# Performance work log

Measured on AMD Instinct MI355X. Metric: run time of the kernel, lower is better.

The kernel has to match this reference:

```python
import jax, jax.numpy as jnp
import numpy as np

B, L = 4, 1024
V, D, H, NL = 32000, 256, 4, 8
S, DC, DI, NTYPES = 16, 4, 512, 5  # d_state, d_conv, d_inner=expand*d_model
NM, NA = 6, 2  # mamba blocks (layers 0,1,2,4,5,6), attention blocks (layers 3,7)


def layernorm(x, g, b):
    m = x.mean(-1, keepdims=True)
    v = x.var(-1, keepdims=True)
    return (x - m) / jnp.sqrt(v + 1e-5) * g + b


def mamba_block(x, g, b, in_w, conv_w, conv_b, xproj_w, dt_w, dt_b, A_log, Dp, out_w):
    res = x
    xn = layernorm(x, g, b)
    xz = xn @ in_w.T                          # [B,L,2*DI]
    xb, z = jnp.split(xz, 2, axis=-1)
    # depthwise causal conv1d (torch pads both sides then truncates to L == left-pad only)
    xc = jnp.transpose(xb, (0, 2, 1))         # [B,DI,L]
    xc = jax.lax.conv_general_dilated(xc, conv_w, (1,), [(DC - 1, 0)], feature_group_count=DI)
    xc = xc + conv_b[None, :, None]
    xb = jax.nn.silu(jnp.transpose(xc, (0, 2, 1)))  # [B,L,DI]
    A = -jnp.exp(A_log)                        # [DI,S]
    Bm, Cm = jnp.split(xb @ xproj_w.T, 2, axis=-1)  # each [B,L,S]
    dt = jax.nn.softplus(xb @ dt_w.T + dt_b)   # [B,L,DI]

    def step(h, inp):
        dt_t, B_t, C_t, x_t = inp              # [B,DI],[B,S],[B,S],[B,DI]
        A_bar = jnp.exp(dt_t[:, :, None] * A)  # [B,DI,S]
        h = A_bar * h + (dt_t * x_t)[:, :, None] * B_t[:, None, :]
        y = (h * C_t[:, None, :]).sum(-1) + Dp * x_t
        return h, y

    h0 = jnp.zeros((x.shape[0], DI, S), x.dtype)
    xs = (jnp.swapaxes(dt, 0, 1), jnp.swapaxes(Bm, 0, 1), jnp.swapaxes(Cm, 0, 1), jnp.swapaxes(xb, 0, 1))
    _, ys = jax.lax.scan(step, h0, xs)         # ys: [L,B,DI]
    y = jnp.swapaxes(ys, 0, 1) * jax.nn.silu(z)
    return y @ out_w.T + res


def attn_block(x, ts, mask, g, b, qkv_w, out_w, decay, ffg, ffb, ff1, ff2):
    Bs, Lq, Dm = x.shape
    dh = Dm // H
    res = x
    xn = layernorm(x, g, b)
    qkv = (xn @ qkv_w.T).reshape(Bs, Lq, 3, H, dh)
    q, k, v = qkv[:, :, 0], qkv[:, :, 1], qkv[:, :, 2]   # [B,L,H,dh]
    attn = jnp.einsum('bqhd,bkhd->bhqk', q, k) * dh ** -0.5
    t_diff = jnp.abs(ts[:, :, None] - ts[:, None, :])[:, None] / 24.0   # [B,1,L,L]
    attn = attn - jax.nn.softplus(decay)[None, :, None, None] * t_diff
    causal = jnp.triu(jnp.ones((Lq, Lq), bool), 1)
    attn = jnp.where(causal[None, None], -jnp.inf, attn)
    attn = jnp.where((mask == 0)[:, None, None, :], -jnp.inf, attn)
    attn = jax.nn.softmax(attn, axis=-1)       # dropout inactive (eval)
    out = jnp.einsum('bhqk,bkhd->bqhd', attn, v).reshape(Bs, Lq, Dm)
    x = res + out @ out_w.T
    xn2 = layernorm(x, ffg, ffb)
    return x + jax.nn.silu(xn2 @ ff1.T) @ ff2.T


def setup_inputs():
    key = jax.random.key(0)
    ks = iter(jax.random.split(key, 64))
    rn = lambda shape, s=0.02: jax.random.normal(next(ks), shape, jnp.float32) * s
    A_init = jnp.log(jnp.tile(jnp.arange(1, S + 1, dtype=jnp.float32)[None, None, :], (NM, DI, 1)))
    return dict(
        token_ids=jax.random.randint(next(ks), (B, L), 0, V, jnp.int32),
        token_types=jax.random.randint(next(ks), (B, L), 0, NTYPES, jnp.int32),
        timestamps=jax.random.uniform(next(ks), (B, L), jnp.float32) * 100.0,
        attention_mask=jnp.ones((B, L), jnp.int32),
        tok_emb=rn((V, D)).at[0].set(0.0),  # padding_idx=0
        type_emb=rn((NTYPES, D)),
        te_freq=rn((D // 2,), 0.01), te_phase=jnp.zeros((D // 2,)),
        te_w=rn((D, D)), te_b=jnp.zeros((D,)),
        m_norm_g=jnp.ones((NM, D)), m_norm_b=jnp.zeros((NM, D)),
        m_in_w=rn((NM, 2 * DI, D)),
        m_conv_w=rn((NM, DI, 1, DC)), m_conv_b=jnp.zeros((NM, DI)),
        m_xproj_w=rn((NM, 2 * S, DI)),
        m_dt_w=rn((NM, DI, DI)), m_dt_b=jnp.zeros((NM, DI)),
        m_Alog=A_init, m_D=jnp.ones((NM, DI)),
        m_out_w=rn((NM, D, DI)),
        a_norm_g=jnp.ones((NA, D)), a_norm_b=jnp.zeros((NA, D)),
        a_qkv_w=rn((NA, 3 * D, D)), a_out_w=rn((NA, D, D)),
        a_decay=jnp.full((NA, H), 0.01, jnp.float32),
        a_ffg=jnp.ones((NA, D)), a_ffb=jnp.zeros((NA, D)),
        a_ff1=rn((NA, 4 * D, D)), a_ff2=rn((NA, D, 4 * D)),
        f_g=jnp.ones((D,)), f_b=jnp.zeros((D,)),
        lm_w=rn((V, D)),
        re_w=rn((1, D)), re_b=jnp.zeros((1,)),
        mo_w=rn((1, D)), mo_b=jnp.zeros((1,)),
    )


def reference(token_ids, token_types, timestamps, attention_mask,
              tok_emb, type_emb, te_freq, te_phase, te_w, te_b,
              m_norm_g, m_norm_b, m_in_w, m_conv_w, m_conv_b, m_xproj_w,
              m_dt_w, m_dt_b, m_Alog, m_D, m_out_w,
              a_norm_g, a_norm_b, a_qkv_w, a_out_w, a_decay, a_ffg, a_ffb, a_ff1, a_ff2,
              f_g, f_b, lm_w, re_w, re_b, mo_w, mo_b):
    t = timestamps[..., None]
    freq = jax.nn.softplus(te_freq)
    enc = jnp.concatenate([jnp.sin(t * freq + te_phase), jnp.cos(t * freq + te_phase)], -1) @ te_w.T + te_b
    x = tok_emb[token_ids] + type_emb[token_types] + enc
    mi = ai = 0
    for i in range(NL):
        if (i + 1) % 4 == 0:
            x = attn_block(x, timestamps, attention_mask,
                           a_norm_g[ai], a_norm_b[ai], a_qkv_w[ai], a_out_w[ai], a_decay[ai],
                           a_ffg[ai], a_ffb[ai], a_ff1[ai], a_ff2[ai])
            ai += 1
        else:
            x = mamba_block(x, m_norm_g[mi], m_norm_b[mi], m_in_w[mi], m_conv_w[mi], m_conv_b[mi],
                            m_xproj_w[mi], m_dt_w[mi], m_dt_b[mi], m_Alog[mi], m_D[mi], m_out_w[mi])
            mi += 1
    x = layernorm(x, f_g, f_b)
    cls = x[:, 0, :]
    lm_logits = x @ lm_w.T
    readm = (cls @ re_w.T + re_b)[:, 0]
    mort = (cls @ mo_w.T + mo_b)[:, 0]
    return lm_logits, readm, mort
```

## Files before the change

kernel.cpp:

```cpp
#include <hip/hip_runtime.h>
#include <hip/hip_bf16.h>
#include <math.h>

#define BB 4
#define LL 1024
#define BL (BB*LL)
#define DD 256
#define VV 32000
#define HH 4
#define DH 64
#define SS 16
#define DCC 4
#define DII 512

typedef float f32x4 __attribute__((ext_vector_type(4)));
typedef short bh8  __attribute__((ext_vector_type(8)));
typedef unsigned short u16;

__device__ __forceinline__ float ex_f(float x) { return __expf(x); }
__device__ __forceinline__ float sp_f(float x) {
    return fmaxf(x, 0.f) + __logf(1.f + __expf(-fabsf(x)));
}
__device__ __forceinline__ float silu_f(float x) {
    return x / (1.f + __expf(-x));
}
__device__ __forceinline__ short f2bf(float f) {
    __hip_bfloat16 h = __float2bfloat16(f);
    short s; __builtin_memcpy(&s, &h, 2); return s;
}
__device__ __forceinline__ float bf2f(u16 u) {
    unsigned v = ((unsigned)u) << 16;
    float f; __builtin_memcpy(&f, &v, 4); return f;
}

#define WB_TOT 5668864
#define LM_TOT 8192000
__global__ void cvtall_k(const float* __restrict__ te_w, const float* __restrict__ a_qkv,
                         const float* __restrict__ a_out, const float* __restrict__ a_ff1,
                         const float* __restrict__ a_ff2, const float* __restrict__ m_in,
                         const float* __restrict__ m_out, const float* __restrict__ m_dt,
                         const float* __restrict__ m_xp, const float* __restrict__ lm,
                         u16* __restrict__ dst, u16* __restrict__ dlm) {
    long i = ((long)blockIdx.x * 256 + threadIdx.x) * 4;
    const float* src; long off; u16* d; long doff;
    if (i >= WB_TOT) {
        long j = i - WB_TOT;
        if (j >= LM_TOT) return;
        src = lm; off = j; d = dlm; doff = j;
    } else {
        d = dst; doff = i;
        if      (i < 65536)   { src = te_w;  off = i; }
        else if (i < 458752)  { src = a_qkv; off = i - 65536; }
        else if (i < 589824)  { src = a_out; off = i - 458752; }
        else if (i < 1114112) { src = a_ff1; off = i - 589824; }
        else if (i < 1638400) { src = a_ff2; off = i - 1114112; }
        else if (i < 3211264) { src = m_in;  off = i - 1638400; }
        else if (i < 3997696) { src = m_out; off = i - 3211264; }
        else {
            long l = i - 3997696;
            int mi = (int)(l / 278528);
            long r = l - (long)mi * 278528;
            if (r < 262144) { src = m_dt + (long)mi * 262144; off = r; }
            else            { src = m_xp + (long)mi * 16384;  off = r - 262144; }
        }
    }
    float4 v = *(const float4*)(src + off);
    ushort4 u;
    u.x = (u16)f2bf(v.x); u.y = (u16)f2bf(v.y);
    u.z = (u16)f2bf(v.z); u.w = (u16)f2bf(v.w);
    *(ushort4*)(d + doff) = u;
}

__global__ void feat_k(const float* __restrict__ ts, const float* __restrict__ freq,
                       const float* __restrict__ phase, u16* __restrict__ feat) {
    int row = blockIdx.x, t = threadIdx.x;
    float tv = ts[row];
    int d = t & 127;
    float f = sp_f(freq[d]);
    float arg = tv * f + phase[d];
    feat[(size_t)row * DD + t] = (u16)f2bf((t < 128) ? sinf(arg) : cosf(arg));
}

__global__ void ln_k(const float* __restrict__ x, const float* __restrict__ g,
                     const float* __restrict__ bbias, u16* __restrict__ out) {
    __shared__ float red[8];
    int row = blockIdx.x, t = threadIdx.x;
    float v = x[(size_t)row * DD + t];
    float s = v;
    #pragma unroll
    for (int o = 32; o >= 1; o >>= 1) s += __shfl_xor(s, o);
    if ((t & 63) == 0) red[t >> 6] = s;
    __syncthreads();
    float mean = (red[0] + red[1] + red[2] + red[3]) * (1.f / 256.f);
    float d = v - mean;
    float s2 = d * d;
    #pragma unroll
    for (int o = 32; o >= 1; o >>= 1) s2 += __shfl_xor(s2, o);
    if ((t & 63) == 0) red[4 + (t >> 6)] = s2;
    __syncthreads();
    float var = (red[4] + red[5] + red[6] + red[7]) * (1.f / 256.f);
    out[(size_t)row * DD + t] = (u16)f2bf(d * rsqrtf(var + 1e-5f) * g[t] + bbias[t]);
}

template <int ACT, bool BOUT, bool VT>
__global__ __launch_bounds__(256) void lngemm_k(
    const float* __restrict__ X, const float* __restrict__ g, const float* __restrict__ bb,
    const u16* __restrict__ W, void* __restrict__ outv, u16* __restrict__ vt,
    int M, int N) {
    __shared__ __align__(16) char Abf[32768];
    __shared__ __align__(16) char Ws[8192];
    __shared__ float gs[256], bs[256];
    int tid = threadIdx.x;
    int bm = blockIdx.y * 64, bn = blockIdx.x * 64;
    gs[tid] = g[tid]; bs[tid] = bb[tid];

    int row = tid >> 2, part = tid & 3;
    const float* xr = X + (size_t)(bm + row) * 256 + part * 64;
    float4 vv[16];
    float s = 0.f, sq = 0.f;
    #pragma unroll
    for (int i = 0; i < 16; ++i) {
        vv[i] = *(const float4*)(xr + i * 4);
        s  += vv[i].x + vv[i].y + vv[i].z + vv[i].w;
        sq += vv[i].x * vv[i].x + vv[i].y * vv[i].y + vv[i].z * vv[i].z + vv[i].w * vv[i].w;
    }
    s += __shfl_xor(s, 1);  s += __shfl_xor(s, 2);
    sq += __shfl_xor(sq, 1); sq += __shfl_xor(sq, 2);
    float mean = s * (1.f / 256.f);
    float rstd = rsqrtf(sq * (1.f / 256.f) - mean * mean + 1e-5f);
    __syncthreads();
    #pragma unroll
    for (int i8 = 0; i8 < 8; ++i8) {
        bh8 p;
        #pragma unroll
        for (int j = 0; j < 8; ++j) {
            int e = i8 * 8 + j;
            float v = (j & 3) == 0 ? vv[e >> 2].x : (j & 3) == 1 ? vv[e >> 2].y
                    : (j & 3) == 2 ? vv[e >> 2].z : vv[e >> 2].w;
            int c = part * 64 + e;
            p[j] = f2bf((v - mean) * rstd * gs[c] + bs[c]);
        }
        *(bh8*)(Abf + (unsigned)((row * 512 + part * 128 + i8 * 16) ^ ((row & 7) << 4))) = p;
    }
    __syncthreads();

    int lane = tid & 63, wv = tid >> 6;
    int wm = wv >> 1, wn = wv & 1;
    int ro = lane & 15, kg = lane >> 4;
    f32x4 acc[2][2];
    #pragma unroll
    for (int i = 0; i < 2; ++i)
        #pragma unroll
        for (int j = 0; j < 2; ++j) acc[i][j] = (f32x4){0.f, 0.f, 0.f, 0.f};

    const u16* gw = W + (size_t)(bn + row) * 256 + part * 16;
    bool wvalid = (bn + row) < N;
    unsigned swb = (unsigned)(row * 128 + part * 32);
    unsigned sx  = (unsigned)((row & 7) << 4);
    for (int kk = 0; kk < 256; kk += 64) {
        if (kk) __syncthreads();
        bh8 w0 = {}, w1 = {};
        if (wvalid) { w0 = *(const bh8*)(gw + kk); w1 = *(const bh8*)(gw + kk + 8); }
        *(bh8*)(Ws + (swb ^ sx)) = w0;
        *(bh8*)(Ws + ((swb + 16) ^ sx)) = w1;
        __syncthreads();
        #pragma unroll
        for (int ks = 0; ks < 2; ++ks) {
            bh8 af[2], bf_[2];
            #pragma unroll
            for (int m = 0; m < 2; ++m) {
                int r = wm * 32 + m * 16 + ro;
                af[m] = *(const bh8*)(Abf + (unsigned)((r * 512 + kk * 2 + ks * 64 + kg * 16) ^ ((r & 7) << 4)));
            }
            #pragma unroll
            for (int n = 0; n < 2; ++n) {
                int r = wn * 32 + n * 16 + ro;
                bf_[n] = *(const bh8*)(Ws + (unsigned)((r * 128 + ks * 64 + kg * 16) ^ ((r & 7) << 4)));
            }
            #pragma unroll
            for (int m = 0; m < 2; ++m)
                #pragma unroll
                for (int n = 0; n < 2; ++n)
                    acc[m][n] = __builtin_amdgcn_mfma_f32_16x16x32_bf16(af[m], bf_[n], acc[m][n], 0, 0, 0);
        }
    }

    float* outf = (float*)outv;
    u16*   outb = (u16*)outv;
    int cr = (lane >> 4) * 4, cc = lane & 15;
    #pragma unroll
    for (int mf = 0; mf < 2; ++mf) {
        #pragma unroll
        for (int nf = 0; nf < 2; ++nf) {
            int n = bn + wn * 32 + nf * 16 + cc;
            if (n >= N) continue;
            int mbase = bm + wm * 32 + mf * 16 + cr;
            f32x4 a = acc[mf][nf];
            #pragma unroll
            for (int r = 0; r < 4; ++r) {
                float v = a[r];
                if (ACT == 1) v = silu_f(v);
                if (BOUT) outb[(size_t)(mbase + r) * N + n] = (u16)f2bf(v);
                else      outf[(size_t)(mbase + r) * N + n] = v;
            }
            if (VT && n >= 512) {
                int hh = (n - 512) >> 6, dd = (n - 512) & 63;
                int b_ = mbase >> 10, l = mbase & 1023;
                ushort4 uv;
                uv.x = (u16)f2bf(acc[mf][nf][0]); uv.y = (u16)f2bf(acc[mf][nf][1]);
                uv.z = (u16)f2bf(acc[mf][nf][2]); uv.w = (u16)f2bf(acc[mf][nf][3]);
                *(ushort4*)(vt + ((((size_t)b_ * HH + hh) * DH + dd) << 10) + l) = uv;
            }
        }
    }
}

template <int ACT, bool HASB, bool HASR, bool BOUT>
__global__ __launch_bounds__(256) void bgemm_k(
    const u16* __restrict__ A, const u16* __restrict__ W,
    const float* __restrict__ bias, const float* __restrict__ res,
    void* __restrict__ outv, float* __restrict__ out2, int M, int N, int K) {
    __shared__ __align__(16) char lds[16384];
    char* As = lds;
    char* Ws = lds + 8192;
    int tid = threadIdx.x;
    int bm = blockIdx.y * 64, bn = blockIdx.x * 64;
    int row = tid >> 2, q = tid & 3;
    int lane = tid & 63, wv = tid >> 6;
    int wm = wv >> 1, wn = wv & 1;
    int ro = lane & 15, kg = lane >> 4;

    f32x4 acc[2][2];
    #pragma unroll
    for (int i = 0; i < 2; ++i)
        #pragma unroll
        for (int j = 0; j < 2; ++j) acc[i][j] = (f32x4){0.f, 0.f, 0.f, 0.f};

    const u16* ga = A + (size_t)(bm + row) * K + q * 16;
    const u16* gw = W + (size_t)(bn + row) * K + q * 16;
    bool wvalid = (bn + row) < N;
    unsigned swb = (unsigned)(row * 128 + q * 32);
    unsigned sx  = (unsigned)((row & 7) << 4);

    for (int kk = 0; kk < K; kk += 64) {
        if (kk) __syncthreads();
        {
            *(bh8*)(As + (swb ^ sx)) = *(const bh8*)(ga);
            *(bh8*)(As + ((swb + 16) ^ sx)) = *(const bh8*)(ga + 8);
            bh8 w0 = {}, w1 = {};
            if (wvalid) { w0 = *(const bh8*)(gw); w1 = *(const bh8*)(gw + 8); }
            *(bh8*)(Ws + (swb ^ sx)) = w0;
            *(bh8*)(Ws + ((swb + 16) ^ sx)) = w1;
        }
        ga += 64; gw += 64;
        __syncthreads();
        #pragma unroll
        for (int ks = 0; ks < 2; ++ks) {
            bh8 af[2], bf_[2];
            #pragma unroll
            for (int m = 0; m < 2; ++m) {
                int r = wm * 32 + m * 16 + ro;
                af[m] = *(const bh8*)(As + (unsigned)((r * 128 + ks * 64 + kg * 16) ^ ((r & 7) << 4)));
            }
            #pragma unroll
            for (int n = 0; n < 2; ++n) {
                int r = wn * 32 + n * 16 + ro;
                bf_[n] = *(const bh8*)(Ws + (unsigned)((r * 128 + ks * 64 + kg * 16) ^ ((r & 7) << 4)));
            }
            #pragma unroll
            for (int m = 0; m < 2; ++m)
                #pragma unroll
                for (int n = 0; n < 2; ++n)
                    acc[m][n] = __builtin_amdgcn_mfma_f32_16x16x32_bf16(af[m], bf_[n], acc[m][n], 0, 0, 0);
        }
    }

    float* outf = (float*)outv;
    u16*   outb = (u16*)outv;
    int cr = (lane >> 4) * 4, cc = lane & 15;
    #pragma unroll
    for (int mf = 0; mf < 2; ++mf) {
        #pragma unroll
        for (int nf = 0; nf < 2; ++nf) {
            int n = bn + wn * 32 + nf * 16 + cc;
            if (n >= N) continue;
            int mbase = bm + wm * 32 + mf * 16 + cr;
            f32x4 a = acc[mf][nf];
            #pragma unroll
            for (int r = 0; r < 4; ++r) {
                float v = a[r];
                int m = mbase + r;
                if (ACT == 3) {
                    if (n < 512) outf[(size_t)m * 512 + n] = sp_f(v + bias[n]);
                    else         out2[(size_t)m * 32 + (n - 512)] = v;
                } else {
                    if (HASB) v += bias[n];
                    if (ACT == 1) v = silu_f(v);
                    if (HASR) v += res[(size_t)m * N + n];
                    if (BOUT) outb[(size_t)m * N + n] = (u16)f2bf(v);
                    else      outf[(size_t)m * N + n] = v;
                }
            }
        }
    }
}

template <int ACT, bool HASB, bool HASR>
__global__ __launch_bounds__(256) void bgemm32_k(
    const u16* __restrict__ A, const u16* __restrict__ W,
    const float* __restrict__ bias, const float* __restrict__ res,
    float* __restrict__ out, int M, int N, int K,
    const int* __restrict__ ids, const int* __restrict__ typ,
    const float* __restrict__ tok, const float* __restrict__ tpe) {
    __shared__ __align__(16) char As[4096];
    __shared__ __align__(16) char Ws[8192];
    int tid = threadIdx.x;
    int bm = blockIdx.y * 32, bn = blockIdx.x * 64;
    int lane = tid & 63, wv = tid >> 6;
    int wm = wv >> 1, wn = wv & 1;
    int ro = lane & 15, kg = lane >> 4;

    f32x4 acc[2];
    acc[0] = (f32x4){0.f, 0.f, 0.f, 0.f};
    acc[1] = (f32x4){0.f, 0.f, 0.f, 0.f};

    int arow = tid >> 3, aq = tid & 7;
    const u16* ga = A + (size_t)(bm + arow) * K + aq * 8;
    unsigned aswb = (unsigned)(arow * 128 + aq * 16);
    unsigned asx  = (unsigned)((arow & 7) << 4);
    int wrow = tid >> 2, wq = tid & 3;
    const u16* gw = W + (size_t)(bn + wrow) * K + wq * 16;
    unsigned wswb = (unsigned)(wrow * 128 + wq * 32);
    unsigned wsx  = (unsigned)((wrow & 7) << 4);

    for (int kk = 0; kk < K; kk += 64) {
        if (kk) __syncthreads();
        *(bh8*)(As + (aswb ^ asx)) = *(const bh8*)(ga);
        *(bh8*)(Ws + (wswb ^ wsx)) = *(const bh8*)(gw);
        *(bh8*)(Ws + ((wswb + 16) ^ wsx)) = *(const bh8*)(gw + 8);
        ga += 64; gw += 64;
        __syncthreads();
        #pragma unroll
        for (int ks = 0; ks < 2; ++ks) {
            int r = wm * 16 + ro;
            bh8 af = *(const bh8*)(As + (unsigned)((r * 128 + ks * 64 + kg * 16) ^ ((r & 7) << 4)));
            #pragma unroll
            for (int n = 0; n < 2; ++n) {
                int rr = wn * 32 + n * 16 + ro;
                bh8 bf_ = *(const bh8*)(Ws + (unsigned)((rr * 128 + ks * 64 + kg * 16) ^ ((rr & 7) << 4)));
                acc[n] = __builtin_amdgcn_mfma_f32_16x16x32_bf16(af, bf_, acc[n], 0, 0, 0);
            }
        }
    }

    int cr = (lane >> 4) * 4, cc = lane & 15;
    #pragma unroll
    for (int nf = 0; nf < 2; ++nf) {
        int n = bn + wn * 32 + nf * 16 + cc;
        int mbase = bm + wm * 16 + cr;
        #pragma unroll
        for (int r = 0; r < 4; ++r) {
            float v = acc[nf][r];
            int m = mbase + r;
            if (ACT == 4) {
                v += bias[n] + tok[(size_t)ids[m] * DD + n] + tpe[(size_t)typ[m] * DD + n];
            } else {
                if (HASB) v += bias[n];
                if (HASR) v += res[(size_t)m * N + n];
            }
            out[(size_t)m * N + n] = v;
        }
    }
}

__global__ __launch_bounds__(256) void mgemmL_k(
    const u16* __restrict__ A, const u16* __restrict__ W,
    float* __restrict__ out, int M, int N, int K) {
    __shared__ __align__(16) char lds[32768];
    char* As = lds;
    char* Ws = lds + 16384;
    int lid = blockIdx.y * 32 + blockIdx.x;
    int xcd = lid & 7, wk = lid >> 3;
    int nt = xcd * 32 + (wk >> 5);
    int mt = wk & 31;
    if (nt * 128 >= N) return;
    int bm = mt * 128, bn = nt * 128;

    int tid = threadIdx.x;
    int row = tid >> 1, half = tid & 1;
    int lane = tid & 63, wv = tid >> 6;
    int wm = wv >> 1, wn = wv & 1;
    int ro = lane & 15, kg = lane >> 4;

    f32x4 acc[4][4];
    #pragma unroll
    for (int i = 0; i < 4; ++i)
        #pragma unroll
        for (int j = 0; j < 4; ++j) acc[i][j] = (f32x4){0.f, 0.f, 0.f, 0.f};

    const u16* ga = A + (size_t)(bm + row) * K + half * 32;
    const u16* gw = W + (size_t)(bn + row) * K + half * 32;
    unsigned swb = (unsigned)(row * 128 + half * 64);
    unsigned sx  = (unsigned)((row & 7) << 4);

    for (int kk = 0; kk < K; kk += 64) {
        if (kk) __syncthreads();
        #pragma unroll
        for (int j = 0; j < 4; ++j) {
            *(bh8*)(As + ((swb + j * 16) ^ sx)) = *(const bh8*)(ga + j * 8);
            *(bh8*)(Ws + ((swb + j * 16) ^ sx)) = *(const bh8*)(gw + j * 8);
        }
        ga += 64; gw += 64;
        __syncthreads();
        #pragma unroll
        for (int ks = 0; ks < 2; ++ks) {
            bh8 af[4], bf_[4];
            #pragma unroll
            for (int m = 0; m < 4; ++m) {
                int r = wm * 64 + m * 16 + ro;
                af[m] = *(const bh8*)(As + (unsigned)((r * 128 + ks * 64 + kg * 16) ^ ((r & 7) << 4)));
            }
            #pragma unroll
            for (int n = 0; n < 4; ++n) {
                int r = wn * 64 + n * 16 + ro;
                bf_[n] = *(const bh8*)(Ws + (unsigned)((r * 128 + ks * 64 + kg * 16) ^ ((r & 7) << 4)));
            }
            #pragma unroll
            for (int m = 0; m < 4; ++m)
                #pragma unroll
                for (int n = 0; n < 4; ++n)
                    acc[m][n] = __builtin_amdgcn_mfma_f32_16x16x32_bf16(af[m], bf_[n], acc[m][n], 0, 0, 0);
        }
    }

    int cr = (lane >> 4) * 4, cc = lane & 15;
    #pragma unroll
    for (int mf = 0; mf < 4; ++mf) {
        #pragma unroll
        for (int nf = 0; nf < 4; ++nf) {
            int n = bn + wn * 64 + nf * 16 + cc;
            int mbase = bm + wm * 64 + mf * 16 + cr;
            f32x4 a = acc[mf][nf];
            #pragma unroll
            for (int r = 0; r < 4; ++r)
                out[(size_t)(mbase + r) * N + n] = a[r];
        }
    }
}

__global__ void conv_k(const u16* __restrict__ xz, const float* __restrict__ w,
                       const float* __restrict__ cb, u16* __restrict__ xbb) {
    int idx = blockIdx.x * blockDim.x + threadIdx.x;
    int c = idx & (DII - 1);
    int row = idx >> 9;
    int l = row & (LL - 1);
    int base = row - l;
    const float* wc = w + c * DCC;
    float s = cb[c];
    #pragma unroll
    for (int j = 0; j < DCC; ++j) {
        int ll = l - (DCC - 1) + j;
        if (ll >= 0) s = fmaf(wc[j], bf2f(xz[((size_t)(base + ll)) * (2 * DII) + c]), s);
    }
    xbb[(size_t)idx] = (u16)f2bf(silu_f(s));
}

__global__ __launch_bounds__(256) void scan_k(
    const float* __restrict__ dt, const u16* __restrict__ xb,
    const float* __restrict__ bc, const u16* __restrict__ xz,
    const float* __restrict__ Alog, const float* __restrict__ Dp,
    u16* __restrict__ y) {
    __shared__ float pa[SS][257];
    __shared__ float ph[SS][257];
    int di = blockIdx.x & (DII - 1);
    int b  = blockIdx.x >> 9;
    int t  = threadIdx.x;
    int l0 = t * 4;
    size_t rb = (size_t)(b * LL + l0);

    float A[SS];
    #pragma unroll
    for (int s = 0; s < SS; ++s) A[s] = -ex_f(Alog[di * SS + s]);

    float dtv[4], xv[4];
    #pragma unroll
    for (int j = 0; j < 4; ++j) {
        dtv[j] = dt[(rb + j) * DII + di];
        xv[j]  = bf2f(xb[(rb + j) * DII + di]);
    }

    float Pa[SS], Ph[SS];
    #pragma unroll
    for (int j = 0; j < 4; ++j) {
        float u = dtv[j] * xv[j];
        const float* bt = bc + (rb + j) * (2 * SS);
        #pragma unroll
        for (int s = 0; s < SS; ++s) {
            float a = ex_f(dtv[j] * A[s]);
            float w = u * bt[s];
            if (j == 0) { Pa[s] = a; Ph[s] = w; }
            else        { Pa[s] *= a; Ph[s] = fmaf(a, Ph[s], w); }
        }
    }
    #pragma unroll
    for (int s = 0; s < SS; ++s) { pa[s][t] = Pa[s]; ph[s][t] = Ph[s]; }
    __syncthreads();

    #pragma unroll
    for (int off = 1; off < 256; off <<= 1) {
        float qa[SS], qh[SS];
        bool has = (t >= off);
        if (has) {
            #pragma unroll
            for (int s = 0; s < SS; ++s) { qa[s] = pa[s][t - off]; qh[s] = ph[s][t - off]; }
        }
        __syncthreads();
        if (has) {
            #pragma unroll
            for (int s = 0; s < SS; ++s) {
                ph[s][t] = fmaf(pa[s][t], qh[s], ph[s][t]);
                pa[s][t] *= qa[s];
            }
        }
        __syncthreads();
    }

    float h[SS];
    if (t == 0) {
        #pragma unroll
        for (int s = 0; s < SS; ++s) h[s] = 0.f;
    } else {
        #pragma unroll
        for (int s = 0; s < SS; ++s) h[s] = ph[s][t - 1];
    }
    float Dv = Dp[di];
    #pragma unroll
    for (int j = 0; j < 4; ++j) {
        float u = dtv[j] * xv[j];
        const float* bt = bc + (rb + j) * (2 * SS);
        float acc = 0.f;
        #pragma unroll
        for (int s = 0; s < SS; ++s) {
            float a = ex_f(dtv[j] * A[s]);
            h[s] = fmaf(a, h[s], u * bt[s]);
            acc = fmaf(h[s], bt[SS + s], acc);
        }
        float zv = bf2f(xz[(rb + j) * (2 * DII) + DII + di]);
        y[(rb + j) * DII + di] = (u16)f2bf(fmaf(Dv, xv[j], acc) * silu_f(zv));
    }
}

__global__ __launch_bounds__(512) void fattn_k(
    const u16* __restrict__ qkv, const u16* __restrict__ vt,
    const float* __restrict__ ts, const int* __restrict__ mask,
    const float* __restrict__ decay, u16* __restrict__ out) {
    __shared__ __align__(16) char ksm[2][8192];
    __shared__ __align__(16) char vsm[2][8192];
    __shared__ __align__(16) char psm[16384];
    __shared__ float mrg[256][25];
    __shared__ float tsk[2][64];
    __shared__ int   msk[2][64];

    int tid = threadIdx.x;
    int grp = tid >> 8;
    int lt  = tid & 255;
    int lane = tid & 63;
    int wvi = (tid >> 6) & 3;
    int qt = blockIdx.x & 15;
    int h  = (blockIdx.x >> 4) & 3;
    int b  = blockIdx.x >> 6;
    int q0 = qt * 64;
    int g = lane >> 4, c = lane & 15;

    bh8 qf[2];
    {
        const u16* qrow = qkv + ((size_t)(b * LL + q0 + wvi * 16 + c)) * (3 * DD) + h * DH;
        qf[0] = *(const bh8*)(qrow + g * 8);
        qf[1] = *(const bh8*)(qrow + 32 + g * 8);
    }
    float tq[4];
    #pragma unroll
    for (int j = 0; j < 4; ++j) tq[j] = ts[b * LL + q0 + wvi * 16 + g * 4 + j];
    float spd = sp_f(decay[h]);

    f32x4 o[4];
    #pragma unroll
    for (int n = 0; n < 4; ++n) o[n] = (f32x4){0.f, 0.f, 0.f, 0.f};
    float mrow[4] = {-INFINITY, -INFINITY, -INFINITY, -INFINITY};
    float drow[4] = {0.f, 0.f, 0.f, 0.f};

    char* pw = psm + (tid >> 6) * 2048;

    int nt = (qt + 2) >> 1;
    for (int it = 0; it < nt; ++it) {
        int kt = it * 2 + grp;
        bool act = (kt <= qt);
        int k0 = kt * 64;
        __syncthreads();
        if (act) {
            int row = lt >> 2, qq = lt & 3;
            unsigned sw = (unsigned)((row & 7) << 4);
            unsigned base = (unsigned)(row * 128 + qq * 32);
            const u16* kr = qkv + ((size_t)(b * LL + k0 + row)) * (3 * DD) + DD + h * DH + qq * 16;
            *(bh8*)(ksm[grp] + (base ^ sw)) = *(const bh8*)(kr);
            *(bh8*)(ksm[grp] + ((base + 16) ^ sw)) = *(const bh8*)(kr + 8);
            const u16* vr = vt + ((((size_t)b * HH + h) * DH + row) << 10) + k0 + qq * 16;
            *(bh8*)(vsm[grp] + (base ^ sw)) = *(const bh8*)(vr);
            *(bh8*)(vsm[grp] + ((base + 16) ^ sw)) = *(const bh8*)(vr + 8);
            if (lt < 64) { tsk[grp][lt] = ts[b * LL + k0 + lt]; msk[grp][lt] = mask[b * LL + k0 + lt]; }
        }
        __syncthreads();
        if (!act) continue;

        f32x4 sf[4];
        #pragma unroll
        for (int n = 0; n < 4; ++n) sf[n] = (f32x4){0.f, 0.f, 0.f, 0.f};
        #pragma unroll
        for (int ks = 0; ks < 2; ++ks) {
            #pragma unroll
            for (int nf = 0; nf < 4; ++nf) {
                int rr = nf * 16 + c;
                bh8 kf = *(const bh8*)(ksm[grp] + (unsigned)((rr * 128 + ks * 64 + g * 16) ^ ((rr & 7) << 4)));
                sf[nf] = __builtin_amdgcn_mfma_f32_16x16x32_bf16(qf[ks], kf, sf[nf], 0, 0, 0);
            }
        }
        float mnew[4] = {mrow[0], mrow[1], mrow[2], mrow[3]};
        #pragma unroll
        for (int nf = 0; nf < 4; ++nf) {
            int kk = c + 16 * nf;
            float tk = tsk[grp][kk];
            bool md = (msk[grp][kk] == 0);
            #pragma unroll
            for (int j = 0; j < 4; ++j) {
                int qrow = q0 + wvi * 16 + g * 4 + j;
                float s = sf[nf][j] * 0.125f - spd * fabsf(tq[j] - tk) * (1.f / 24.f);
                bool dead = md || (k0 + kk > qrow);
                s = dead ? -INFINITY : s;
                sf[nf][j] = s;
                mnew[j] = fmaxf(mnew[j], s);
            }
        }
        #pragma unroll
        for (int off = 1; off <= 8; off <<= 1)
            #pragma unroll
            for (int j = 0; j < 4; ++j) mnew[j] = fmaxf(mnew[j], __shfl_xor(mnew[j], off));
        float scl[4], psum[4];
        #pragma unroll
        for (int j = 0; j < 4; ++j) {
            scl[j] = (mnew[j] == -INFINITY) ? 1.f : ex_f(mrow[j] - mnew[j]);
            psum[j] = 0.f;
            mrow[j] = mnew[j];
        }
        #pragma unroll
        for (int nf = 0; nf < 4; ++nf) {
            #pragma unroll
            for (int j = 0; j < 4; ++j) {
                float s = sf[nf][j];
                float p = (s == -INFINITY) ? 0.f : ex_f(s - mrow[j]);
                psum[j] += p;
                int row = g * 4 + j;
                *(short*)(pw + (unsigned)((row * 128 + (c + 16 * nf) * 2) ^ ((row & 7) << 4))) = f2bf(p);
            }
        }
        #pragma unroll
        for (int off = 1; off <= 8; off <<= 1)
            #pragma unroll
            for (int j = 0; j < 4; ++j) psum[j] += __shfl_xor(psum[j], off);
        #pragma unroll
        for (int j = 0; j < 4; ++j) drow[j] = drow[j] * scl[j] + psum[j];
        #pragma unroll
        for (int n = 0; n < 4; ++n)
            #pragma unroll
            for (int j = 0; j < 4; ++j) o[n][j] *= scl[j];
        #pragma unroll
        for (int ks = 0; ks < 2; ++ks) {
            bh8 pf = *(const bh8*)(pw + (unsigned)((c * 128 + ks * 64 + g * 16) ^ ((c & 7) << 4)));
            #pragma unroll
            for (int n = 0; n < 4; ++n) {
                int rr = n * 16 + c;
                bh8 vf = *(const bh8*)(vsm[grp] + (unsigned)((rr * 128 + ks * 64 + g * 16) ^ ((rr & 7) << 4)));
                o[n] = __builtin_amdgcn_mfma_f32_16x16x32_bf16(pf, vf, o[n], 0, 0, 0);
            }
        }
    }

    __syncthreads();
    if (grp == 1) {
        float* m_ = mrg[lt];
        #pragma unroll
        for (int j = 0; j < 4; ++j) { m_[j] = mrow[j]; m_[4 + j] = drow[j]; }
        #pragma unroll
        for (int n = 0; n < 4; ++n)
            #pragma unroll
            for (int j = 0; j < 4; ++j) m_[8 + n * 4 + j] = o[n][j];
    }
    __syncthreads();
    if (grp == 0) {
        float* m_ = mrg[lt];
        #pragma unroll
        for (int j = 0; j < 4; ++j) {
            float m1 = m_[j], d1 = m_[4 + j];
            float mm = fmaxf(mrow[j], m1);
            float s0 = (mrow[j] == -INFINITY) ? 0.f : ex_f(mrow[j] - mm);
            float s1 = (m1 == -INFINITY) ? 0.f : ex_f(m1 - mm);
            drow[j] = drow[j] * s0 + d1 * s1;
            #pragma unroll
            for (int n = 0; n < 4; ++n)
                o[n][j] = o[n][j] * s0 + m_[8 + n * 4 + j] * s1;
        }
        #pragma unroll
        for (int n = 0; n < 4; ++n) {
            #pragma unroll
            for (int j = 0; j < 4; ++j) {
                int qrow = q0 + wvi * 16 + g * 4 + j;
                out[((size_t)(b * LL + qrow)) * DD + h * DH + c + 16 * n] = (u16)f2bf(o[n][j] / drow[j]);
            }
        }
    }
}

__global__ __launch_bounds__(64) void heads_k(
    const u16* __restrict__ xn, const float* __restrict__ re_w, const float* __restrict__ re_b,
    const float* __restrict__ mo_w, const float* __restrict__ mo_b, float* __restrict__ out) {
    int lane = threadIdx.x;
    int b = blockIdx.x & 3;
    int which = blockIdx.x >> 2;
    const float* wv = which ? mo_w : re_w;
    const u16* row = xn + (size_t)b * LL * DD;
    float s = 0.f;
    #pragma unroll
    for (int d = 0; d < DD / 64; ++d) s = fmaf(bf2f(row[lane + d * 64]), wv[lane + d * 64], s);
    #pragma unroll
    for (int o = 32; o >= 1; o >>= 1) s += __shfl_xor(s, o);
    if (lane == 0) out[(size_t)VV * BL + which * 4 + b] = s + (which ? mo_b[0] : re_b[0]);
}

extern "C" void kernel_launch(void* const* d_in, const int* in_sizes, int n_in,
                              void* d_out, int out_size, void* d_ws, size_t ws_size,
                              hipStream_t stream) {
    const int*   ids      = (const int*)  d_in[0];
    const int*   typ      = (const int*)  d_in[1];
    const float* ts       = (const float*)d_in[2];
    const int*   amask    = (const int*)  d_in[3];
    const float* tok_emb  = (const float*)d_in[4];
    const float* type_emb = (const float*)d_in[5];
    const float* te_freq  = (const float*)d_in[6];
    const float* te_phase = (const float*)d_in[7];
    const float* te_w     = (const float*)d_in[8];
    const float* te_b     = (const float*)d_in[9];
    const float* m_norm_g = (const float*)d_in[10];
    const float* m_norm_b = (const float*)d_in[11];
    const float* m_in_w   = (const float*)d_in[12];
    const float* m_conv_w = (const float*)d_in[13];
    const float* m_conv_b = (const float*)d_in[14];
    const float* m_xproj  = (const float*)d_in[15];
    const float* m_dt_w   = (const float*)d_in[16];
    const float* m_dt_b   = (const float*)d_in[17];
    const float* m_Alog   = (const float*)d_in[18];
    const float* m_D      = (const float*)d_in[19];
    const float* m_out_w  = (const float*)d_in[20];
    const float* a_norm_g = (const float*)d_in[21];
    const float* a_norm_b = (const float*)d_in[22];
    const float* a_qkv_w  = (const float*)d_in[23];
    const float* a_out_w  = (const float*)d_in[24];
    const float* a_decay  = (const float*)d_in[25];
    const float* a_ffg    = (const float*)d_in[26];
    const float* a_ffb    = (const float*)d_in[27];
    const float* a_ff1    = (const float*)d_in[28];
    const float* a_ff2    = (const float*)d_in[29];
    const float* f_g      = (const float*)d_in[30];
    const float* f_b      = (const float*)d_in[31];
    const float* lm_w     = (const float*)d_in[32];
    const float* re_w     = (const float*)d_in[33];
    const float* re_b     = (const float*)d_in[34];
    const float* mo_w     = (const float*)d_in[35];
    const float* mo_b     = (const float*)d_in[36];

    float* out = (float*)d_out;
    float* ws  = (float*)d_ws;

    float* x    = ws;
    u16*   xnb  = (u16*)(ws + 1048576);
    u16*   t1   = (u16*)(ws + 1572864);
    u16*   b1   = (u16*)(ws + 3670016);
    u16*   b2   = (u16*)(ws + 5767168);
    float* t3   = ws + 6815744;
    float* t5   = ws + 8912896;
    u16*   vtb  = (u16*)(ws + 9043968);
    u16*   wbuf = (u16*)(ws + 9568256);
    u16*   wlm  = (u16*)(ws + 12402688);

    const u16* w_te  = wbuf;
    const u16* w_qkv = wbuf + 65536;
    const u16* w_ao  = wbuf + 458752;
    const u16* w_ff1 = wbuf + 589824;
    const u16* w_ff2 = wbuf + 1114112;
    const u16* w_min = wbuf + 1638400;
    const u16* w_mo  = wbuf + 3211264;
    const u16* w_dtx = wbuf + 3997696;

    cvtall_k<<<(WB_TOT + LM_TOT) / 1024, 256, 0, stream>>>(
        te_w, a_qkv_w, a_out_w, a_ff1, a_ff2, m_in_w, m_out_w, m_dt_w, m_xproj, lm_w, wbuf, wlm);
    feat_k<<<BL, 256, 0, stream>>>(ts, te_freq, te_phase, b1);
    bgemm32_k<4, true, false><<<dim3(4, BL / 32), 256, 0, stream>>>(
        b1, w_te, te_b, nullptr, x, BL, DD, DD, ids, typ, tok_emb, type_emb);

    int mi = 0, ai = 0;
    for (int i = 0; i < 8; ++i) {
        if ((i + 1) % 4 == 0) {
            lngemm_k<0, true, true><<<dim3(12, BL / 64), 256, 0, stream>>>(
                x, a_norm_g + ai * DD, a_norm_b + ai * DD,
                w_qkv + (size_t)ai * 196608, t1, vtb, BL, 3 * DD);
            fattn_k<<<BB * HH * (LL / 64), 512, 0, stream>>>(
                t1, vtb, ts, amask, a_decay + ai * HH, b1);
            bgemm32_k<0, false, true><<<dim3(4, BL / 32), 256, 0, stream>>>(
                b1, w_ao + (size_t)ai * 65536, nullptr, x, x, BL, DD, DD,
                nullptr, nullptr, nullptr, nullptr);
            lngemm_k<1, true, false><<<dim3(16, BL / 64), 256, 0, stream>>>(
                x, a_ffg + ai * DD, a_ffb + ai * DD,
                w_ff1 + (size_t)ai * 262144, b1, nullptr, BL, 4 * DD);
            bgemm32_k<0, false, true><<<dim3(4, BL / 32), 256, 0, stream>>>(
                b1, w_ff2 + (size_t)ai * 262144, nullptr, x, x, BL, DD, 4 * DD,
                nullptr, nullptr, nullptr, nullptr);
            ++ai;
        } else {
            lngemm_k<0, true, false><<<dim3(16, BL / 64), 256, 0, stream>>>(
                x, m_norm_g + mi * DD, m_norm_b + mi * DD,
                w_min + (size_t)mi * 262144, t1, nullptr, BL, 2 * DII);
            conv_k<<<(BL * DII) / 256, 256, 0, stream>>>(
                t1, m_conv_w + (size_t)mi * DII * DCC, m_conv_b + mi * DII, b1);
            bgemm_k<3, true, false, false><<<dim3(9, BL / 64), 256, 0, stream>>>(
                b1, w_dtx + (size_t)mi * 278528, m_dt_b + mi * DII, nullptr, t3, t5, BL, 544, DII);
            scan_k<<<BB * DII, 256, 0, stream>>>(
                t3, b1, t5, t1, m_Alog + (size_t)mi * DII * SS, m_D + mi * DII, b2);
            bgemm32_k<0, false, true><<<dim3(4, BL / 32), 256, 0, stream>>>(
                b2, w_mo + (size_t)mi * 131072, nullptr, x, x, BL, DD, DII,
                nullptr, nullptr, nullptr, nullptr);
            ++mi;
        }
    }

    ln_k<<<BL, 256, 0, stream>>>(x, f_g, f_b, xnb);
    mgemmL_k<<<dim3(32, 256), 256, 0, stream>>>(xnb, wlm, out, BL, VV, DD);
    heads_k<<<8, 64, 0, stream>>>(xnb, re_w, re_b, mo_w, mo_b, out);
}
```

Measured before the change: 1.171 ms.

## Replace shared-memory block scan with wavefront shuffle scan plus cross-wave carry

```diff
diff --git a/kernel.cpp b/kernel.cpp
--- a/kernel.cpp
+++ b/kernel.cpp
@@ -470,11 +470,12 @@
     const float* __restrict__ bc, const u16* __restrict__ xz,
     const float* __restrict__ Alog, const float* __restrict__ Dp,
     u16* __restrict__ y) {
-    __shared__ float pa[SS][257];
-    __shared__ float ph[SS][257];
+    __shared__ float wta[4][SS];
+    __shared__ float wtb[4][SS];
     int di = blockIdx.x & (DII - 1);
     int b  = blockIdx.x >> 9;
     int t  = threadIdx.x;
+    int lane = t & 63, wvi = t >> 6;
     int l0 = t * 4;
     size_t rb = (size_t)(b * LL + l0);
 
@@ -502,37 +503,47 @@
             else        { Pa[s] *= a; Ph[s] = fmaf(a, Ph[s], w); }
         }
     }
-    #pragma unroll
-    for (int s = 0; s < SS; ++s) { pa[s][t] = Pa[s]; ph[s][t] = Ph[s]; }
+
+    #pragma unroll
+    for (int off = 1; off <= 32; off <<= 1) {
+        float qa[SS], qh[SS];
+        #pragma unroll
+        for (int s = 0; s < SS; ++s) {
+            qa[s] = __shfl_up(Pa[s], off);
+            qh[s] = __shfl_up(Ph[s], off);
+        }
+        if (lane >= off) {
+            #pragma unroll
+            for (int s = 0; s < SS; ++s) {
+                Ph[s] = fmaf(Pa[s], qh[s], Ph[s]);
+                Pa[s] *= qa[s];
+            }
+        }
+    }
+    if (lane == 63) {
+        #pragma unroll
+        for (int s = 0; s < SS; ++s) { wta[wvi][s] = Pa[s]; wtb[wvi][s] = Ph[s]; }
+    }
     __syncthreads();
-
-    #pragma unroll
-    for (int off = 1; off < 256; off <<= 1) {
-        float qa[SS], qh[SS];
-        bool has = (t >= off);
-        if (has) {
-            #pragma unroll
-            for (int s = 0; s < SS; ++s) { qa[s] = pa[s][t - off]; qh[s] = ph[s][t - off]; }
-        }
-        __syncthreads();
-        if (has) {
-            #pragma unroll
-            for (int s = 0; s < SS; ++s) {
-                ph[s][t] = fmaf(pa[s][t], qh[s], ph[s][t]);
-                pa[s][t] *= qa[s];
-            }
-        }
-        __syncthreads();
-    }
+    float Wb[SS];
+    #pragma unroll
+    for (int s = 0; s < SS; ++s) Wb[s] = 0.f;
+    for (int w = 0; w < wvi; ++w) {
+        #pragma unroll
+        for (int s = 0; s < SS; ++s)
+            Wb[s] = fmaf(wta[w][s], Wb[s], wtb[w][s]);
+    }
+    float Fb[SS];
+    #pragma unroll
+    for (int s = 0; s < SS; ++s) Fb[s] = fmaf(Pa[s], Wb[s], Ph[s]);
 
     float h[SS];
-    if (t == 0) {
-        #pragma unroll
-        for (int s = 0; s < SS; ++s) h[s] = 0.f;
-    } else {
-        #pragma unroll
-        for (int s = 0; s < SS; ++s) h[s] = ph[s][t - 1];
-    }
+    #pragma unroll
+    for (int s = 0; s < SS; ++s) {
+        float up = __shfl_up(Fb[s], 1);
+        h[s] = (lane == 0) ? ((wvi == 0) ? 0.f : Wb[s]) : up;
+    }
+
     float Dv = Dp[di];
     #pragma unroll
     for (int j = 0; j < 4; ++j) {
```

Result: slower. 1.196 ms (+2.1%).
